# Kernel optimization log

Measured on AMD Instinct MI355X. Metric: run time of the kernel, lower is better.

The kernel has to match this reference:

```python
import jax, jax.numpy as jnp
import numpy as np

BN_EPS = 1e-5
L2_EPS = 1e-8


def l2norm(x, axis=-1):
    # matches torch: x / (sqrt(sum(x^2)) + eps)
    n = jnp.sqrt(jnp.sum(x * x, axis=axis, keepdims=True)) + L2_EPS
    return x / n


def setup_inputs() -> dict:
    key = jax.random.key(0)
    ks = jax.random.split(key, 8)
    B, N, D, E = 512, 193, 512, 2048
    g = 4                      # uniform pid-group size (<= max_rows=8)
    k_tok = (N - 1) // 2       # = 96, matches DynamicLinearProjection k
    H = E // 2                 # MLP hidden = 1024
    base_features = jax.random.normal(ks[0], (B, N, D), jnp.float32)
    atten = jax.random.uniform(ks[1], (B, N, N), jnp.float32)
    pid = jnp.arange(B) // g   # contiguous groups of size g
    # dynamic projection params for group size g
    W_dyn = jax.random.normal(ks[2], (g, D), jnp.float32)          # weights[f'weight_{g}'] ~ randn
    b_dyn = jnp.zeros((g,), jnp.float32)
    W_lin = jax.random.normal(ks[3], (E, k_tok * g), jnp.float32) * 0.02  # linears[f'linear_{g}']
    b_lin = jnp.zeros((E,), jnp.float32)
    # MLP(input=512, hidden=1024, output=2048, 2 layers)
    W1 = jax.random.normal(ks[4], (H, D), jnp.float32) * 0.02
    b1 = jnp.zeros((H,), jnp.float32)
    gamma1 = jnp.ones((H,), jnp.float32)
    beta1 = jnp.zeros((H,), jnp.float32)
    W2 = jax.random.normal(ks[5], (E, H), jnp.float32) * 0.02
    b2 = jnp.zeros((E,), jnp.float32)
    return {"base_features": base_features, "atten": atten, "pid": pid,
            "W_dyn": W_dyn, "b_dyn": b_dyn, "W_lin": W_lin, "b_lin": b_lin,
            "W1": W1, "b1": b1, "gamma1": gamma1, "beta1": beta1,
            "W2": W2, "b2": b2}


def reference(base_features, atten, pid, W_dyn, b_dyn, W_lin, b_lin,
              W1, b1, gamma1, beta1, W2, b2):
    B, N, D = base_features.shape
    k_tok = (N - 1) // 2                      # 96
    g = W_dyn.shape[0]                        # uniform group size (pid = arange//g)
    G = B // g
    E = W_lin.shape[0]
    # --- top-k token selection (atten[:, :, 0] = -1, then topk over atten[:, 0, :]) ---
    scores = atten[:, 0, :].at[:, 0].set(-1.0)            # (B, N)
    _, idx = jax.lax.top_k(scores, k_tok)                 # (B, k_tok), descending
    feats = jnp.take_along_axis(base_features, idx[:, :, None], axis=1)  # (B, k_tok, D)
    # --- per-pid-group dynamic projection (uniform groups -> one batched GEMM) ---
    # torch: cat group members -> (g*k_tok, D); F.linear(x, W_dyn, b_dyn).T -> (g, g*k_tok); linear_g -> (g, E)
    Xg = feats.reshape(G, g * k_tok, D)
    y = jnp.einsum('gnd,rd->grn', Xg, W_dyn) + b_dyn[None, :, None]     # (G, g, g*k_tok)
    new_feats = jnp.einsum('gri,oi->gro', y, W_lin) + b_lin             # (G, g, E)
    # scatter: output[member_idx] = row; contiguous groups => plain reshape
    new_feats = l2norm(new_feats.reshape(B, E))
    # --- MLP branch on l2-normalized selected features ---
    x = l2norm(feats).reshape(B * k_tok, D)
    h = x @ W1.T + b1
    mu = jnp.mean(h, axis=0)
    var = jnp.var(h, axis=0)                  # biased, as torch BN training-mode
    h = (h - mu) * jax.lax.rsqrt(var + BN_EPS) * gamma1 + beta1
    h = jax.nn.relu(h)
    out = (h @ W2.T + b2).reshape(B, k_tok, E)
    pooled = jnp.max(out, axis=1)             # maxk_pool1d_var with k=1 => max over tokens
    return (pooled + new_feats).astype(jnp.float32)
```

## Files before the change

kernel.cpp:

```cpp
#include <hip/hip_runtime.h>
#include <math.h>

#define B_   512
#define N_   193
#define D_   512
#define E_   2048
#define KTOK 96
#define H_   1024
#define M1   (B_ * KTOK)
#define KGD  (KTOK * 4)

typedef _Float16 half8 __attribute__((ext_vector_type(8)));
typedef _Float16 half4v __attribute__((ext_vector_type(4)));
typedef float floatx4 __attribute__((ext_vector_type(4)));

__device__ __forceinline__ void gll16(const _Float16* g, _Float16* l) {
    __builtin_amdgcn_global_load_lds(
        (const __attribute__((address_space(1))) unsigned int*)(const void*)g,
        (__attribute__((address_space(3))) unsigned int*)(void*)l, 16, 0, 0);
}

__global__ void zero_stats_kernel(double* stats) {
    int i = blockIdx.x * 256 + threadIdx.x;
    if (i < 2 * H_) stats[i] = 0.0;
}

__global__ void topk_kernel(const float* __restrict__ atten, int* __restrict__ idx) {
    __shared__ float s[N_];
    int b = blockIdx.x;
    const float* row = atten + (size_t)b * N_ * N_;
    for (int i = threadIdx.x; i < N_; i += blockDim.x)
        s[i] = (i == 0) ? -1.0f : row[i];
    __syncthreads();
    for (int i = threadIdx.x; i < N_; i += blockDim.x) {
        float v = s[i];
        int rank = 0;
        for (int j = 0; j < N_; ++j) {
            float u = s[j];
            rank += (u > v) || (u == v && j < i);
        }
        if (rank < KTOK) idx[b * KTOK + rank] = i;
    }
}

__global__ __launch_bounds__(256) void gather_kernel(
        const float* __restrict__ base, const int* __restrict__ idx,
        const float* __restrict__ W_dyn, const float* __restrict__ b_dyn,
        _Float16* __restrict__ Xh, float* __restrict__ Y) {
    int ln = threadIdx.x & 63, wv = threadIdx.x >> 6;
    int rowid = blockIdx.x * 4 + wv;
    int b = rowid / KTOK, t = rowid - b * KTOK;
    int tok = idx[rowid];
    const float4* src = (const float4*)(base + ((size_t)b * N_ + tok) * D_);
    float4 v0 = src[ln * 2], v1 = src[ln * 2 + 1];

    float vals[5];
    vals[0] = v0.x * v0.x + v0.y * v0.y + v0.z * v0.z + v0.w * v0.w
            + v1.x * v1.x + v1.y * v1.y + v1.z * v1.z + v1.w * v1.w;
#pragma unroll
    for (int r = 0; r < 4; ++r) {
        const float4* wr = (const float4*)(W_dyn + r * D_);
        float4 w0 = wr[ln * 2], w1 = wr[ln * 2 + 1];
        vals[1 + r] = v0.x * w0.x + v0.y * w0.y + v0.z * w0.z + v0.w * w0.w
                    + v1.x * w1.x + v1.y * w1.y + v1.z * w1.z + v1.w * w1.w;
    }
#pragma unroll
    for (int c = 0; c < 5; ++c)
#pragma unroll
        for (int o = 32; o > 0; o >>= 1) vals[c] += __shfl_xor(vals[c], o, 64);

    float inv = 1.0f / (sqrtf(vals[0]) + 1e-8f);
    half8 o8;
    o8[0] = (_Float16)(v0.x * inv); o8[1] = (_Float16)(v0.y * inv);
    o8[2] = (_Float16)(v0.z * inv); o8[3] = (_Float16)(v0.w * inv);
    o8[4] = (_Float16)(v1.x * inv); o8[5] = (_Float16)(v1.y * inv);
    o8[6] = (_Float16)(v1.z * inv); o8[7] = (_Float16)(v1.w * inv);
    *(half8*)&Xh[(size_t)rowid * D_ + ln * 8] = o8;
    if (ln == 0) {
        int g = b >> 2;
        int n = (b & 3) * KTOK + t;
#pragma unroll
        for (int r = 0; r < 4; ++r)
            Y[(size_t)(g * 4 + r) * KGD + n] = vals[1 + r] + b_dyn[r];
    }
}

__global__ __launch_bounds__(256) void newfeat_kernel(
        const float* __restrict__ Y, const float* __restrict__ W_lin,
        const float* __restrict__ b_lin, float* __restrict__ NF) {
    __shared__ float sy[4][KGD];
    __shared__ float red[4][4];
    __shared__ float tot[4];
    int b0 = blockIdx.x * 4;
    int tid = threadIdx.x;
    for (int l = tid; l < 4 * KGD; l += 256)
        sy[l / KGD][l % KGD] = Y[(size_t)b0 * KGD + l];
    __syncthreads();

    float out[4][8];
    float ssq[4] = {0.f, 0.f, 0.f, 0.f};
#pragma unroll
    for (int q = 0; q < 8; ++q) {
        int o = tid + 256 * q;
        float a0 = 0.f, a1 = 0.f, a2 = 0.f, a3 = 0.f;
        const float4* wr = (const float4*)(W_lin + (size_t)o * KGD);
        for (int i4 = 0; i4 < KGD / 4; ++i4) {
            float4 w  = wr[i4];
            float4 s0 = *(const float4*)&sy[0][i4 * 4];
            float4 s1 = *(const float4*)&sy[1][i4 * 4];
            float4 s2 = *(const float4*)&sy[2][i4 * 4];
            float4 s3 = *(const float4*)&sy[3][i4 * 4];
            a0 += w.x * s0.x + w.y * s0.y + w.z * s0.z + w.w * s0.w;
            a1 += w.x * s1.x + w.y * s1.y + w.z * s1.z + w.w * s1.w;
            a2 += w.x * s2.x + w.y * s2.y + w.z * s2.z + w.w * s2.w;
            a3 += w.x * s3.x + w.y * s3.y + w.z * s3.z + w.w * s3.w;
        }
        float bl = b_lin[o];
        out[0][q] = a0 + bl; out[1][q] = a1 + bl;
        out[2][q] = a2 + bl; out[3][q] = a3 + bl;
#pragma unroll
        for (int r = 0; r < 4; ++r) ssq[r] += out[r][q] * out[r][q];
    }

    int lane = tid & 63, wid = tid >> 6;
#pragma unroll
    for (int c = 0; c < 4; ++c) {
        float v = ssq[c];
        for (int o = 32; o > 0; o >>= 1) v += __shfl_down(v, o, 64);
        if (lane == 0) red[c][wid] = v;
    }
    __syncthreads();
    if (tid < 4) tot[tid] = red[tid][0] + red[tid][1] + red[tid][2] + red[tid][3];
    __syncthreads();
#pragma unroll
    for (int r = 0; r < 4; ++r) {
        float norm = sqrtf(tot[r]) + 1e-8f;
#pragma unroll
        for (int q = 0; q < 8; ++q) {
            int o = tid + 256 * q;
            NF[(size_t)(b0 + r) * E_ + o] = out[r][q] / norm;
        }
    }
}

__global__ __launch_bounds__(256) void convw_kernel(
        const float* __restrict__ W1, const float* __restrict__ W2,
        _Float16* __restrict__ W1h, _Float16* __restrict__ W2h) {
    int i = blockIdx.x * 256 + threadIdx.x;
    if (i < 131072) {
        float4 v = *(const float4*)&W1[(size_t)i * 4];
        half4v o = {(_Float16)v.x, (_Float16)v.y, (_Float16)v.z, (_Float16)v.w};
        *(half4v*)&W1h[(size_t)i * 4] = o;
    } else {
        int j = i - 131072;
        float4 v = *(const float4*)&W2[(size_t)j * 4];
        half4v o = {(_Float16)v.x, (_Float16)v.y, (_Float16)v.z, (_Float16)v.w};
        *(half4v*)&W2h[(size_t)j * 4] = o;
    }
}

__global__ __launch_bounds__(512, 2) void gemm1s(
        const _Float16* __restrict__ A, const _Float16* __restrict__ Bm,
        const float* __restrict__ bias, _Float16* __restrict__ Cf16,
        double* __restrict__ stats) {
    constexpr int KA = 512, NS = 16, NBX = 4;
    __shared__ _Float16 Sl[4][14336];
    int tid = threadIdx.x;
    int ln = tid & 63, w = tid >> 6;
    int wr = w >> 2, wc = w & 3;
    int rid = blockIdx.x;
    int q = rid >> 3;
    int bx = q & (NBX - 1);
    int by = ((q / NBX) << 3) | (rid & 7);
    int n0 = bx * 256, m0 = by * 192;

    bool isA = (w < 4);
    const _Float16* sg[4];
    int ld[4];
    if (isA) {
#pragma unroll
        for (int i = 0; i < 3; ++i) {
            int j = w * 3 + i;
            int u = j * 64 + ln;
            int kg = u / 192, row = u - kg * 192;
            sg[i] = A + (size_t)(m0 + row) * KA + kg * 8;
            ld[i] = j * 512;
        }
        sg[3] = sg[0]; ld[3] = ld[0];
    } else {
#pragma unroll
        for (int i = 0; i < 4; ++i) {
            int j = (w - 4) * 4 + i;
            int u = j * 64 + ln;
            int kg = u >> 8, col = u & 255;
            sg[i] = Bm + (size_t)(n0 + col) * KA + kg * 8;
            ld[i] = 6144 + j * 512;
        }
    }

#define CSTAGE(s) { int ko = (s) * 32; _Float16* dst = &Sl[(s) & 3][0];        \
    if (isA) { gll16(sg[0] + ko, dst + ld[0]); gll16(sg[1] + ko, dst + ld[1]); \
               gll16(sg[2] + ko, dst + ld[2]); }                               \
    else     { gll16(sg[0] + ko, dst + ld[0]); gll16(sg[1] + ko, dst + ld[1]); \
               gll16(sg[2] + ko, dst + ld[2]); gll16(sg[3] + ko, dst + ld[3]); } }
#define WAITV(na, nb) { if (isA) asm volatile("s_waitcnt vmcnt(" #na ")" ::: "memory"); \
                        else     asm volatile("s_waitcnt vmcnt(" #nb ")" ::: "memory"); }

    int aofs[6], bofs[4];
#pragma unroll
    for (int f = 0; f < 6; ++f)
        aofs[f] = ((ln >> 4) * 192 + wr * 96 + f * 16 + (ln & 15)) * 8;
#pragma unroll
    for (int n = 0; n < 4; ++n)
        bofs[n] = 6144 + ((ln >> 4) * 256 + wc * 64 + n * 16 + (ln & 15)) * 8;

    floatx4 zero = {0.f, 0.f, 0.f, 0.f};
    floatx4 acc[6][4];
#pragma unroll
    for (int i = 0; i < 6; ++i)
#pragma unroll
        for (int j = 0; j < 4; ++j) acc[i][j] = zero;

    CSTAGE(0); CSTAGE(1); CSTAGE(2);
    WAITV(6, 8);
    __builtin_amdgcn_s_barrier();

    for (int s = 0; s < NS; ++s) {
        const _Float16* SL = &Sl[s & 3][0];
        half8 bv[4], av[3];
#pragma unroll
        for (int n = 0; n < 4; ++n) bv[n] = *(const half8*)&SL[bofs[n]];
#pragma unroll
        for (int f = 0; f < 3; ++f) av[f] = *(const half8*)&SL[aofs[f]];
        if (s + 3 < NS) CSTAGE(s + 3);
        __builtin_amdgcn_sched_barrier(0);
        __builtin_amdgcn_s_barrier();
        asm volatile("s_waitcnt lgkmcnt(0)" ::: "memory");
        __builtin_amdgcn_sched_barrier(0);
        __builtin_amdgcn_s_setprio(1);
#pragma unroll
        for (int f = 0; f < 3; ++f)
#pragma unroll
            for (int n = 0; n < 4; ++n)
                acc[f][n] = __builtin_amdgcn_mfma_f32_16x16x32_f16(av[f], bv[n], acc[f][n], 0, 0, 0);
        __builtin_amdgcn_s_setprio(0);
        __builtin_amdgcn_sched_barrier(0);
        __builtin_amdgcn_s_barrier();
        half8 av2[3];
#pragma unroll
        for (int f = 0; f < 3; ++f) av2[f] = *(const half8*)&SL[aofs[3 + f]];
        __builtin_amdgcn_sched_barrier(0);
        if (s + 1 < NS) {
            if (s + 3 < NS)      { WAITV(6, 8); }
            else if (s + 2 < NS) { WAITV(3, 4); }
            else                 { WAITV(0, 0); }
        }
        __builtin_amdgcn_s_barrier();
        asm volatile("s_waitcnt lgkmcnt(0)" ::: "memory");
        __builtin_amdgcn_sched_barrier(0);
        __builtin_amdgcn_s_setprio(1);
#pragma unroll
        for (int f = 0; f < 3; ++f)
#pragma unroll
            for (int n = 0; n < 4; ++n)
                acc[3 + f][n] = __builtin_amdgcn_mfma_f32_16x16x32_f16(av2[f], bv[n], acc[3 + f][n], 0, 0, 0);
        __builtin_amdgcn_s_setprio(0);
        __builtin_amdgcn_sched_barrier(0);
        __builtin_amdgcn_s_barrier();
    }
#undef CSTAGE
#undef WAITV

    float cs[4] = {0.f, 0.f, 0.f, 0.f}, cq[4] = {0.f, 0.f, 0.f, 0.f};
#pragma unroll
    for (int f = 0; f < 6; ++f) {
        int row = m0 + wr * 96 + f * 16 + (ln >> 4) * 4;
#pragma unroll
        for (int n = 0; n < 4; ++n) {
            int col = n0 + wc * 64 + n * 16 + (ln & 15);
            float bb = bias[col];
#pragma unroll
            for (int r = 0; r < 4; ++r) {
                float v = acc[f][n][r] + bb;
                Cf16[(size_t)(row + r) * H_ + col] = (_Float16)v;
                cs[n] += v; cq[n] += v * v;
            }
        }
    }
#pragma unroll
    for (int n = 0; n < 4; ++n) {
        cs[n] += __shfl_xor(cs[n], 16); cs[n] += __shfl_xor(cs[n], 32);
        cq[n] += __shfl_xor(cq[n], 16); cq[n] += __shfl_xor(cq[n], 32);
    }
    float* sp = (float*)&Sl[0][0];
    if (ln < 16) {
#pragma unroll
        for (int n = 0; n < 4; ++n) {
            int c = wc * 64 + n * 16 + ln;
            sp[(wr * 256 + c) * 2 + 0] = cs[n];
            sp[(wr * 256 + c) * 2 + 1] = cq[n];
        }
    }
    __syncthreads();
    if (tid < 256) {
        float s0 = sp[tid * 2]     + sp[(256 + tid) * 2];
        float q0 = sp[tid * 2 + 1] + sp[(256 + tid) * 2 + 1];
        atomicAdd(&stats[n0 + tid], (double)s0);
        atomicAdd(&stats[H_ + n0 + tid], (double)q0);
    }
}

__global__ void finalize_kernel(const double* __restrict__ stats,
                                const float* __restrict__ gamma,
                                const float* __restrict__ beta,
                                _Float16* __restrict__ scsh16) {
    int c = blockIdx.x * 256 + threadIdx.x;
    if (c >= H_) return;
    double mean = stats[c] / (double)M1;
    double var  = stats[H_ + c] / (double)M1 - mean * mean;
    float sc = gamma[c] * (float)(1.0 / sqrt(var + 1e-5));
    float sh = beta[c] - (float)mean * sc;
    scsh16[c] = (_Float16)sc;
    scsh16[H_ + c] = (_Float16)sh;
}

__device__ __forceinline__ half8 bnrelu8(half8 h, const _Float16* scp, const _Float16* shp) {
    half8 s = *(const half8*)scp, t = *(const half8*)shp, o;
#pragma unroll
    for (int e = 0; e < 8; ++e) {
        float v = (float)h[e] * (float)s[e] + (float)t[e];
        o[e] = (_Float16)fmaxf(v, 0.f);
    }
    return o;
}

__global__ __launch_bounds__(512, 2) void gemm2f(
        const _Float16* __restrict__ Hb, const _Float16* __restrict__ Bm,
        const _Float16* __restrict__ scsh16, const float* __restrict__ bias,
        const float* __restrict__ NF, float* __restrict__ out) {
    constexpr int KA = 1024, NS = 32, NBX = 8;
    __shared__ _Float16 Sl[4][14336];
    __shared__ _Float16 scL[H_], shL[H_];
    int tid = threadIdx.x;
    int ln = tid & 63, w = tid >> 6;
    int wr = w >> 2, wc = w & 3;
    int rid = blockIdx.x;
    int qq = rid >> 3;
    int bx = qq & (NBX - 1);
    int by = ((qq / NBX) << 3) | (rid & 7);
    int n0 = bx * 256, m0 = by * 192;
    bool isA = (w < 4);

    for (int i = tid; i < H_; i += 512) { scL[i] = scsh16[i]; shL[i] = scsh16[H_ + i]; }

    const _Float16 *sgA0 = Hb, *sgA1 = Hb, *sgA2 = Hb;
    int ldA0 = 0, ldA1 = 0, ldA2 = 0, kgA0 = 0, kgA1 = 0, kgA2 = 0;
    const _Float16* sgB[4] = {Bm, Bm, Bm, Bm};
    int ldB[4] = {6144, 6144, 6144, 6144};
    if (isA) {
        { int j = w * 3 + 0; int u = j * 64 + ln; kgA0 = u / 192; int row = u - kgA0 * 192;
          sgA0 = Hb + (size_t)(m0 + row) * KA + kgA0 * 8; ldA0 = j * 512; }
        { int j = w * 3 + 1; int u = j * 64 + ln; kgA1 = u / 192; int row = u - kgA1 * 192;
          sgA1 = Hb + (size_t)(m0 + row) * KA + kgA1 * 8; ldA1 = j * 512; }
        { int j = w * 3 + 2; int u = j * 64 + ln; kgA2 = u / 192; int row = u - kgA2 * 192;
          sgA2 = Hb + (size_t)(m0 + row) * KA + kgA2 * 8; ldA2 = j * 512; }
    } else {
#pragma unroll
        for (int i = 0; i < 4; ++i) {
            int j = (w - 4) * 4 + i;
            int u = j * 64 + ln;
            int kg = u >> 8, col = u & 255;
            sgB[i] = Bm + (size_t)(n0 + col) * KA + kg * 8;
            ldB[i] = 6144 + j * 512;
        }
    }

#define A_ISSUE(t, Ra, Rb, Rc) { Ra = *(const half8*)(sgA0 + (size_t)(t) * 32); \
    Rb = *(const half8*)(sgA1 + (size_t)(t) * 32);                              \
    Rc = *(const half8*)(sgA2 + (size_t)(t) * 32); }
#define A_XFRM(t, Ra, Rb, Rc) { _Float16* dst = &Sl[(t) & 3][0]; int c0 = (t) * 32; \
    *(half8*)(dst + ldA0 + ln * 8) = bnrelu8(Ra, &scL[c0 + kgA0 * 8], &shL[c0 + kgA0 * 8]); \
    *(half8*)(dst + ldA1 + ln * 8) = bnrelu8(Rb, &scL[c0 + kgA1 * 8], &shL[c0 + kgA1 * 8]); \
    *(half8*)(dst + ldA2 + ln * 8) = bnrelu8(Rc, &scL[c0 + kgA2 * 8], &shL[c0 + kgA2 * 8]); }
#define B_STAGE(t) { int ko = (t) * 32; _Float16* dst = &Sl[(t) & 3][0]; \
    gll16(sgB[0] + ko, dst + ldB[0]); gll16(sgB[1] + ko, dst + ldB[1]); \
    gll16(sgB[2] + ko, dst + ldB[2]); gll16(sgB[3] + ko, dst + ldB[3]); }

    int aofs[6], bofs[4];
#pragma unroll
    for (int f = 0; f < 6; ++f)
        aofs[f] = ((ln >> 4) * 192 + wr * 96 + f * 16 + (ln & 15)) * 8;
#pragma unroll
    for (int n = 0; n < 4; ++n)
        bofs[n] = 6144 + ((ln >> 4) * 256 + wc * 64 + n * 16 + (ln & 15)) * 8;

    floatx4 zero = {0.f, 0.f, 0.f, 0.f};
    floatx4 acc[6][4];
#pragma unroll
    for (int i = 0; i < 6; ++i)
#pragma unroll
        for (int j = 0; j < 4; ++j) acc[i][j] = zero;

    half8 e0a, e0b, e0c, e1a, e1b, e1c;

    if (isA) { A_ISSUE(0, e0a, e0b, e0c); A_ISSUE(1, e1a, e1b, e1c); }
    else     { B_STAGE(0); B_STAGE(1); B_STAGE(2); }
    asm volatile("s_waitcnt lgkmcnt(0)" ::: "memory");
    __builtin_amdgcn_s_barrier();
    if (isA) {
        A_XFRM(0, e0a, e0b, e0c);
        A_ISSUE(2, e0a, e0b, e0c);
        A_XFRM(1, e1a, e1b, e1c);
    } else {
        asm volatile("s_waitcnt vmcnt(8)" ::: "memory");
    }
    asm volatile("s_waitcnt lgkmcnt(0)" ::: "memory");
    __builtin_amdgcn_s_barrier();

#define SLOT(s, Ia, Ib, Ic, Xa, Xb, Xc) {                                       \
    const _Float16* SL = &Sl[(s) & 3][0];                                       \
    half8 bv[4], av[3], av2[3];                                                 \
    _Pragma("unroll") for (int n = 0; n < 4; ++n) bv[n] = *(const half8*)&SL[bofs[n]]; \
    _Pragma("unroll") for (int f = 0; f < 3; ++f) av[f] = *(const half8*)&SL[aofs[f]]; \
    if ((s) + 3 < NS) { if (isA) { A_ISSUE((s) + 3, Ia, Ib, Ic); } else { B_STAGE((s) + 3); } } \
    __builtin_amdgcn_sched_barrier(0);                                          \
    __builtin_amdgcn_s_barrier();                                               \
    asm volatile("s_waitcnt lgkmcnt(0)" ::: "memory");                          \
    __builtin_amdgcn_sched_barrier(0);                                          \
    __builtin_amdgcn_s_setprio(1);                                              \
    _Pragma("unroll") for (int f = 0; f < 3; ++f)                               \
        _Pragma("unroll") for (int n = 0; n < 4; ++n)                           \
            acc[f][n] = __builtin_amdgcn_mfma_f32_16x16x32_f16(av[f], bv[n], acc[f][n], 0, 0, 0); \
    __builtin_amdgcn_s_setprio(0);                                              \
    __builtin_amdgcn_sched_barrier(0);                                          \
    __builtin_amdgcn_s_barrier();                                               \
    _Pragma("unroll") for (int f = 0; f < 3; ++f) av2[f] = *(const half8*)&SL[aofs[3 + f]]; \
    __builtin_amdgcn_sched_barrier(0);                                          \
    __builtin_amdgcn_s_barrier();                                               \
    asm volatile("s_waitcnt lgkmcnt(0)" ::: "memory");                          \
    __builtin_amdgcn_sched_barrier(0);                                          \
    __builtin_amdgcn_s_setprio(1);                                              \
    _Pragma("unroll") for (int f = 0; f < 3; ++f)                               \
        _Pragma("unroll") for (int n = 0; n < 4; ++n)                           \
            acc[3 + f][n] = __builtin_amdgcn_mfma_f32_16x16x32_f16(av2[f], bv[n], acc[3 + f][n], 0, 0, 0); \
    __builtin_amdgcn_s_setprio(0);                                              \
    __builtin_amdgcn_sched_barrier(0);                                          \
    if (isA) {                                                                  \
        if ((s) + 2 < NS) { A_XFRM((s) + 2, Xa, Xb, Xc); }                      \
    } else {                                                                    \
        if ((s) + 3 < NS)      { asm volatile("s_waitcnt vmcnt(8)" ::: "memory"); } \
        else if ((s) + 2 < NS) { asm volatile("s_waitcnt vmcnt(4)" ::: "memory"); } \
        else if ((s) + 1 < NS) { asm volatile("s_waitcnt vmcnt(0)" ::: "memory"); } \
    }                                                                           \
    __builtin_amdgcn_s_barrier();                                               \
}

    for (int s = 0; s < NS; s += 2) {
        SLOT(s,     e1a, e1b, e1c, e0a, e0b, e0c);
        SLOT(s + 1, e0a, e0b, e0c, e1a, e1b, e1c);
    }
#undef SLOT
#undef A_ISSUE
#undef A_XFRM
#undef B_STAGE

    int batch = by * 2 + wr;
#pragma unroll
    for (int n = 0; n < 4; ++n) {
        float m = -3.4e38f;
#pragma unroll
        for (int f = 0; f < 6; ++f)
#pragma unroll
            for (int r = 0; r < 4; ++r) m = fmaxf(m, acc[f][n][r]);
        m = fmaxf(m, __shfl_xor(m, 16));
        m = fmaxf(m, __shfl_xor(m, 32));
        if (ln < 16) {
            int col = n0 + wc * 64 + n * 16 + ln;
            out[(size_t)batch * E_ + col] = m + bias[col] + NF[(size_t)batch * E_ + col];
        }
    }
}

extern "C" void kernel_launch(void* const* d_in, const int* in_sizes, int n_in,
                              void* d_out, int out_size, void* d_ws, size_t ws_size,
                              hipStream_t stream) {
    (void)in_sizes; (void)n_in; (void)out_size; (void)ws_size;
    const float* base  = (const float*)d_in[0];
    const float* atten = (const float*)d_in[1];
    const float* W_dyn = (const float*)d_in[3];
    const float* b_dyn = (const float*)d_in[4];
    const float* W_lin = (const float*)d_in[5];
    const float* b_lin = (const float*)d_in[6];
    const float* W1    = (const float*)d_in[7];
    const float* b1    = (const float*)d_in[8];
    const float* gamma = (const float*)d_in[9];
    const float* beta  = (const float*)d_in[10];
    const float* W2    = (const float*)d_in[11];
    const float* b2    = (const float*)d_in[12];
    float* out = (float*)d_out;

    char* wsp = (char*)d_ws;
    int*      idx    = (int*)(wsp);
    float*    Y      = (float*)(wsp + 196608);
    float*    NF     = (float*)(wsp + 983040);
    double*   stats  = (double*)(wsp + 5177344);
    _Float16* scsh16 = (_Float16*)(wsp + 5193728);
    _Float16* W1h    = (_Float16*)(wsp + 5201920);
    _Float16* W2h    = (_Float16*)(wsp + 6250496);
    _Float16* Xh     = (_Float16*)(wsp + 10444800);
    _Float16* Hbh    = (_Float16*)(wsp + 60776448);

    zero_stats_kernel<<<8, 256, 0, stream>>>(stats);
    topk_kernel<<<B_, 256, 0, stream>>>(atten, idx);
    convw_kernel<<<2560, 256, 0, stream>>>(W1, W2, W1h, W2h);
    gather_kernel<<<M1 / 4, 256, 0, stream>>>(base, idx, W_dyn, b_dyn, Xh, Y);
    newfeat_kernel<<<B_ / 4, 256, 0, stream>>>(Y, W_lin, b_lin, NF);
    gemm1s<<<1024, 512, 0, stream>>>(Xh, W1h, b1, Hbh, stats);
    finalize_kernel<<<4, 256, 0, stream>>>(stats, gamma, beta, scsh16);
    gemm2f<<<2048, 512, 0, stream>>>(Hbh, W2h, scsh16, b2, NF, out);
}
```

Measured before the change: 542.0 us.

## Switch both GEMMs to double-buffered BK=64 stages with all-warp loading

Both GEMM kernels move from a 4-slot, 32-wide K pipeline with three stages in flight to a 2-slot, 64-wide K double buffer. In gemm1s all warps now share the global-to-LDS loads rather than splitting them into A-loader and B-loader warps. Each iteration runs two MFMA halves with fewer barriers, so there is less synchronisation per K step. The cost is a shallower prefetch: each iteration ends with a full vmcnt(0) wait, which may expose global memory latency.

```diff
diff --git a/kernel.cpp b/kernel.cpp
--- a/kernel.cpp
+++ b/kernel.cpp
@@ -159,12 +159,13 @@
     }
 }
 
+
 __global__ __launch_bounds__(512, 2) void gemm1s(
         const _Float16* __restrict__ A, const _Float16* __restrict__ Bm,
         const float* __restrict__ bias, _Float16* __restrict__ Cf16,
         double* __restrict__ stats) {
-    constexpr int KA = 512, NS = 16, NBX = 4;
-    __shared__ _Float16 Sl[4][14336];
+    constexpr int KA = 512, NS = 8, NBX = 4;
+    __shared__ _Float16 Sl[2][28672];
     int tid = threadIdx.x;
     int ln = tid & 63, w = tid >> 6;
     int wr = w >> 2, wc = w & 3;
@@ -174,45 +175,37 @@
     int by = ((q / NBX) << 3) | (rid & 7);
     int n0 = bx * 256, m0 = by * 192;
 
-    bool isA = (w < 4);
-    const _Float16* sg[4];
-    int ld[4];
-    if (isA) {
-#pragma unroll
-        for (int i = 0; i < 3; ++i) {
-            int j = w * 3 + i;
-            int u = j * 64 + ln;
+    const _Float16* sg[7];
+    int ld[7];
+#pragma unroll
+    for (int i = 0; i < 7; ++i) {
+        int c = w * 7 + i;
+        if (c < 24) {
+            int u = c * 64 + ln;
             int kg = u / 192, row = u - kg * 192;
             sg[i] = A + (size_t)(m0 + row) * KA + kg * 8;
-            ld[i] = j * 512;
-        }
-        sg[3] = sg[0]; ld[3] = ld[0];
-    } else {
-#pragma unroll
-        for (int i = 0; i < 4; ++i) {
-            int j = (w - 4) * 4 + i;
-            int u = j * 64 + ln;
+            ld[i] = c * 512;
+        } else {
+            int u = (c - 24) * 64 + ln;
             int kg = u >> 8, col = u & 255;
             sg[i] = Bm + (size_t)(n0 + col) * KA + kg * 8;
-            ld[i] = 6144 + j * 512;
-        }
-    }
-
-#define CSTAGE(s) { int ko = (s) * 32; _Float16* dst = &Sl[(s) & 3][0];        \
-    if (isA) { gll16(sg[0] + ko, dst + ld[0]); gll16(sg[1] + ko, dst + ld[1]); \
-               gll16(sg[2] + ko, dst + ld[2]); }                               \
-    else     { gll16(sg[0] + ko, dst + ld[0]); gll16(sg[1] + ko, dst + ld[1]); \
-               gll16(sg[2] + ko, dst + ld[2]); gll16(sg[3] + ko, dst + ld[3]); } }
-#define WAITV(na, nb) { if (isA) asm volatile("s_waitcnt vmcnt(" #na ")" ::: "memory"); \
-                        else     asm volatile("s_waitcnt vmcnt(" #nb ")" ::: "memory"); }
-
-    int aofs[6], bofs[4];
+            ld[i] = 12288 + (c - 24) * 512;
+        }
+    }
+#define G1STAGE(t) { int ko = (t) * 64; _Float16* dst = &Sl[(t) & 1][0];      \
+    _Pragma("unroll") for (int i = 0; i < 7; ++i) gll16(sg[i] + ko, dst + ld[i]); }
+
+    int aofs[6][2], bofs[4][2];
 #pragma unroll
     for (int f = 0; f < 6; ++f)
-        aofs[f] = ((ln >> 4) * 192 + wr * 96 + f * 16 + (ln & 15)) * 8;
+#pragma unroll
+        for (int h = 0; h < 2; ++h)
+            aofs[f][h] = ((h * 4 + (ln >> 4)) * 192 + wr * 96 + f * 16 + (ln & 15)) * 8;
 #pragma unroll
     for (int n = 0; n < 4; ++n)
-        bofs[n] = 6144 + ((ln >> 4) * 256 + wc * 64 + n * 16 + (ln & 15)) * 8;
+#pragma unroll
+        for (int h = 0; h < 2; ++h)
+            bofs[n][h] = 12288 + ((h * 4 + (ln >> 4)) * 256 + wc * 64 + n * 16 + (ln & 15)) * 8;
 
     floatx4 zero = {0.f, 0.f, 0.f, 0.f};
     floatx4 acc[6][4];
@@ -221,55 +214,48 @@
 #pragma unroll
         for (int j = 0; j < 4; ++j) acc[i][j] = zero;
 
-    CSTAGE(0); CSTAGE(1); CSTAGE(2);
-    WAITV(6, 8);
+    G1STAGE(0);
+    asm volatile("s_waitcnt vmcnt(0)" ::: "memory");
     __builtin_amdgcn_s_barrier();
 
     for (int s = 0; s < NS; ++s) {
-        const _Float16* SL = &Sl[s & 3][0];
-        half8 bv[4], av[3];
-#pragma unroll
-        for (int n = 0; n < 4; ++n) bv[n] = *(const half8*)&SL[bofs[n]];
-#pragma unroll
-        for (int f = 0; f < 3; ++f) av[f] = *(const half8*)&SL[aofs[f]];
-        if (s + 3 < NS) CSTAGE(s + 3);
-        __builtin_amdgcn_sched_barrier(0);
-        __builtin_amdgcn_s_barrier();
+        const _Float16* SL = &Sl[s & 1][0];
+        half8 a0[6], b0[4];
+#pragma unroll
+        for (int n = 0; n < 4; ++n) b0[n] = *(const half8*)&SL[bofs[n][0]];
+#pragma unroll
+        for (int f = 0; f < 6; ++f) a0[f] = *(const half8*)&SL[aofs[f][0]];
+        if (s + 1 < NS) G1STAGE(s + 1);
         asm volatile("s_waitcnt lgkmcnt(0)" ::: "memory");
         __builtin_amdgcn_sched_barrier(0);
         __builtin_amdgcn_s_setprio(1);
 #pragma unroll
-        for (int f = 0; f < 3; ++f)
+        for (int f = 0; f < 6; ++f)
 #pragma unroll
             for (int n = 0; n < 4; ++n)
-                acc[f][n] = __builtin_amdgcn_mfma_f32_16x16x32_f16(av[f], bv[n], acc[f][n], 0, 0, 0);
+                acc[f][n] = __builtin_amdgcn_mfma_f32_16x16x32_f16(a0[f], b0[n], acc[f][n], 0, 0, 0);
         __builtin_amdgcn_s_setprio(0);
+        {
+            half8 a1[6], b1[4];
+#pragma unroll
+            for (int n = 0; n < 4; ++n) b1[n] = *(const half8*)&SL[bofs[n][1]];
+#pragma unroll
+            for (int f = 0; f < 6; ++f) a1[f] = *(const half8*)&SL[aofs[f][1]];
+            asm volatile("s_waitcnt lgkmcnt(0)" ::: "memory");
+            __builtin_amdgcn_sched_barrier(0);
+            __builtin_amdgcn_s_setprio(1);
+#pragma unroll
+            for (int f = 0; f < 6; ++f)
+#pragma unroll
+                for (int n = 0; n < 4; ++n)
+                    acc[f][n] = __builtin_amdgcn_mfma_f32_16x16x32_f16(a1[f], b1[n], acc[f][n], 0, 0, 0);
+            __builtin_amdgcn_s_setprio(0);
+        }
         __builtin_amdgcn_sched_barrier(0);
+        asm volatile("s_waitcnt vmcnt(0)" ::: "memory");
         __builtin_amdgcn_s_barrier();
-        half8 av2[3];
-#pragma unroll
-        for (int f = 0; f < 3; ++f) av2[f] = *(const half8*)&SL[aofs[3 + f]];
-        __builtin_amdgcn_sched_barrier(0);
-        if (s + 1 < NS) {
-            if (s + 3 < NS)      { WAITV(6, 8); }
-            else if (s + 2 < NS) { WAITV(3, 4); }
-            else                 { WAITV(0, 0); }
-        }
-        __builtin_amdgcn_s_barrier();
-        asm volatile("s_waitcnt lgkmcnt(0)" ::: "memory");
-        __builtin_amdgcn_sched_barrier(0);
-        __builtin_amdgcn_s_setprio(1);
-#pragma unroll
-        for (int f = 0; f < 3; ++f)
-#pragma unroll
-            for (int n = 0; n < 4; ++n)
-                acc[3 + f][n] = __builtin_amdgcn_mfma_f32_16x16x32_f16(av2[f], bv[n], acc[3 + f][n], 0, 0, 0);
-        __builtin_amdgcn_s_setprio(0);
-        __builtin_amdgcn_sched_barrier(0);
-        __builtin_amdgcn_s_barrier();
-    }
-#undef CSTAGE
-#undef WAITV
+    }
+#undef G1STAGE
 
     float cs[4] = {0.f, 0.f, 0.f, 0.f}, cq[4] = {0.f, 0.f, 0.f, 0.f};
 #pragma unroll
@@ -338,8 +324,8 @@
         const _Float16* __restrict__ Hb, const _Float16* __restrict__ Bm,
         const _Float16* __restrict__ scsh16, const float* __restrict__ bias,
         const float* __restrict__ NF, float* __restrict__ out) {
-    constexpr int KA = 1024, NS = 32, NBX = 8;
-    __shared__ _Float16 Sl[4][14336];
+    constexpr int KA = 1024, NS = 16, NBX = 8;
+    __shared__ _Float16 Sl[2][28672];
     __shared__ _Float16 scL[H_], shL[H_];
     int tid = threadIdx.x;
     int ln = tid & 63, w = tid >> 6;
@@ -353,46 +339,53 @@
 
     for (int i = tid; i < H_; i += 512) { scL[i] = scsh16[i]; shL[i] = scsh16[H_ + i]; }
 
-    const _Float16 *sgA0 = Hb, *sgA1 = Hb, *sgA2 = Hb;
-    int ldA0 = 0, ldA1 = 0, ldA2 = 0, kgA0 = 0, kgA1 = 0, kgA2 = 0;
-    const _Float16* sgB[4] = {Bm, Bm, Bm, Bm};
-    int ldB[4] = {6144, 6144, 6144, 6144};
+    const _Float16* sgA[6];
+    int ldA[6], cgA[6];
+    half8 ar[6];
     if (isA) {
-        { int j = w * 3 + 0; int u = j * 64 + ln; kgA0 = u / 192; int row = u - kgA0 * 192;
-          sgA0 = Hb + (size_t)(m0 + row) * KA + kgA0 * 8; ldA0 = j * 512; }
-        { int j = w * 3 + 1; int u = j * 64 + ln; kgA1 = u / 192; int row = u - kgA1 * 192;
-          sgA1 = Hb + (size_t)(m0 + row) * KA + kgA1 * 8; ldA1 = j * 512; }
-        { int j = w * 3 + 2; int u = j * 64 + ln; kgA2 = u / 192; int row = u - kgA2 * 192;
-          sgA2 = Hb + (size_t)(m0 + row) * KA + kgA2 * 8; ldA2 = j * 512; }
-    } else {
-#pragma unroll
-        for (int i = 0; i < 4; ++i) {
-            int j = (w - 4) * 4 + i;
-            int u = j * 64 + ln;
+#pragma unroll
+        for (int i = 0; i < 6; ++i) {
+            int c = w * 6 + i;
+            int u = c * 64 + ln;
+            int kg = u / 192, row = u - kg * 192;
+            sgA[i] = Hb + (size_t)(m0 + row) * KA + kg * 8;
+            ldA[i] = c * 512;
+            cgA[i] = kg;
+        }
+    }
+    const _Float16* sgB[8];
+    int ldB[8];
+    if (!isA) {
+#pragma unroll
+        for (int i = 0; i < 8; ++i) {
+            int c = (w - 4) * 8 + i;
+            int u = c * 64 + ln;
             int kg = u >> 8, col = u & 255;
             sgB[i] = Bm + (size_t)(n0 + col) * KA + kg * 8;
-            ldB[i] = 6144 + j * 512;
-        }
-    }
-
-#define A_ISSUE(t, Ra, Rb, Rc) { Ra = *(const half8*)(sgA0 + (size_t)(t) * 32); \
-    Rb = *(const half8*)(sgA1 + (size_t)(t) * 32);                              \
-    Rc = *(const half8*)(sgA2 + (size_t)(t) * 32); }
-#define A_XFRM(t, Ra, Rb, Rc) { _Float16* dst = &Sl[(t) & 3][0]; int c0 = (t) * 32; \
-    *(half8*)(dst + ldA0 + ln * 8) = bnrelu8(Ra, &scL[c0 + kgA0 * 8], &shL[c0 + kgA0 * 8]); \
-    *(half8*)(dst + ldA1 + ln * 8) = bnrelu8(Rb, &scL[c0 + kgA1 * 8], &shL[c0 + kgA1 * 8]); \
-    *(half8*)(dst + ldA2 + ln * 8) = bnrelu8(Rc, &scL[c0 + kgA2 * 8], &shL[c0 + kgA2 * 8]); }
-#define B_STAGE(t) { int ko = (t) * 32; _Float16* dst = &Sl[(t) & 3][0]; \
-    gll16(sgB[0] + ko, dst + ldB[0]); gll16(sgB[1] + ko, dst + ldB[1]); \
-    gll16(sgB[2] + ko, dst + ldB[2]); gll16(sgB[3] + ko, dst + ldB[3]); }
-
-    int aofs[6], bofs[4];
+            ldB[i] = 12288 + c * 512;
+        }
+    }
+
+#define A_ISSUE(t) { _Pragma("unroll") for (int i = 0; i < 6; ++i)            \
+    ar[i] = *(const half8*)(sgA[i] + (size_t)(t) * 64); }
+#define A_XFRM(t) { _Float16* dst = &Sl[(t) & 1][0];                          \
+    _Pragma("unroll") for (int i = 0; i < 6; ++i) {                           \
+        int c0 = (t) * 64 + cgA[i] * 8;                                       \
+        *(half8*)(dst + ldA[i] + ln * 8) = bnrelu8(ar[i], &scL[c0], &shL[c0]); } }
+#define B_STAGE(t) { int ko = (t) * 64; _Float16* dst = &Sl[(t) & 1][0];      \
+    _Pragma("unroll") for (int i = 0; i < 8; ++i) gll16(sgB[i] + ko, dst + ldB[i]); }
+
+    int aofs[6][2], bofs[4][2];
 #pragma unroll
     for (int f = 0; f < 6; ++f)
-        aofs[f] = ((ln >> 4) * 192 + wr * 96 + f * 16 + (ln & 15)) * 8;
+#pragma unroll
+        for (int h = 0; h < 2; ++h)
+            aofs[f][h] = ((h * 4 + (ln >> 4)) * 192 + wr * 96 + f * 16 + (ln & 15)) * 8;
 #pragma unroll
     for (int n = 0; n < 4; ++n)
-        bofs[n] = 6144 + ((ln >> 4) * 256 + wc * 64 + n * 16 + (ln & 15)) * 8;
+#pragma unroll
+        for (int h = 0; h < 2; ++h)
+            bofs[n][h] = 12288 + ((h * 4 + (ln >> 4)) * 256 + wc * 64 + n * 16 + (ln & 15)) * 8;
 
     floatx4 zero = {0.f, 0.f, 0.f, 0.f};
     floatx4 acc[6][4];
@@ -401,65 +394,51 @@
 #pragma unroll
         for (int j = 0; j < 4; ++j) acc[i][j] = zero;
 
-    half8 e0a, e0b, e0c, e1a, e1b, e1c;
-
-    if (isA) { A_ISSUE(0, e0a, e0b, e0c); A_ISSUE(1, e1a, e1b, e1c); }
-    else     { B_STAGE(0); B_STAGE(1); B_STAGE(2); }
+    if (isA) { A_ISSUE(0); } else { B_STAGE(0); }
     asm volatile("s_waitcnt lgkmcnt(0)" ::: "memory");
     __builtin_amdgcn_s_barrier();
-    if (isA) {
-        A_XFRM(0, e0a, e0b, e0c);
-        A_ISSUE(2, e0a, e0b, e0c);
-        A_XFRM(1, e1a, e1b, e1c);
-    } else {
-        asm volatile("s_waitcnt vmcnt(8)" ::: "memory");
-    }
-    asm volatile("s_waitcnt lgkmcnt(0)" ::: "memory");
+    if (isA) { A_XFRM(0); }
+    asm volatile("s_waitcnt lgkmcnt(0) vmcnt(0)" ::: "memory");
     __builtin_amdgcn_s_barrier();
 
-#define SLOT(s, Ia, Ib, Ic, Xa, Xb, Xc) {                                       \
-    const _Float16* SL = &Sl[(s) & 3][0];                                       \
-    half8 bv[4], av[3], av2[3];                                                 \
-    _Pragma("unroll") for (int n = 0; n < 4; ++n) bv[n] = *(const half8*)&SL[bofs[n]]; \
-    _Pragma("unroll") for (int f = 0; f < 3; ++f) av[f] = *(const half8*)&SL[aofs[f]]; \
-    if ((s) + 3 < NS) { if (isA) { A_ISSUE((s) + 3, Ia, Ib, Ic); } else { B_STAGE((s) + 3); } } \
-    __builtin_amdgcn_sched_barrier(0);                                          \
-    __builtin_amdgcn_s_barrier();                                               \
-    asm volatile("s_waitcnt lgkmcnt(0)" ::: "memory");                          \
-    __builtin_amdgcn_sched_barrier(0);                                          \
-    __builtin_amdgcn_s_setprio(1);                                              \
-    _Pragma("unroll") for (int f = 0; f < 3; ++f)                               \
-        _Pragma("unroll") for (int n = 0; n < 4; ++n)                           \
-            acc[f][n] = __builtin_amdgcn_mfma_f32_16x16x32_f16(av[f], bv[n], acc[f][n], 0, 0, 0); \
-    __builtin_amdgcn_s_setprio(0);                                              \
-    __builtin_amdgcn_sched_barrier(0);                                          \
-    __builtin_amdgcn_s_barrier();                                               \
-    _Pragma("unroll") for (int f = 0; f < 3; ++f) av2[f] = *(const half8*)&SL[aofs[3 + f]]; \
-    __builtin_amdgcn_sched_barrier(0);                                          \
-    __builtin_amdgcn_s_barrier();                                               \
-    asm volatile("s_waitcnt lgkmcnt(0)" ::: "memory");                          \
-    __builtin_amdgcn_sched_barrier(0);                                          \
-    __builtin_amdgcn_s_setprio(1);                                              \
-    _Pragma("unroll") for (int f = 0; f < 3; ++f)                               \
-        _Pragma("unroll") for (int n = 0; n < 4; ++n)                           \
-            acc[3 + f][n] = __builtin_amdgcn_mfma_f32_16x16x32_f16(av2[f], bv[n], acc[3 + f][n], 0, 0, 0); \
-    __builtin_amdgcn_s_setprio(0);                                              \
-    __builtin_amdgcn_sched_barrier(0);                                          \
-    if (isA) {                                                                  \
-        if ((s) + 2 < NS) { A_XFRM((s) + 2, Xa, Xb, Xc); }                      \
-    } else {                                                                    \
-        if ((s) + 3 < NS)      { asm volatile("s_waitcnt vmcnt(8)" ::: "memory"); } \
-        else if ((s) + 2 < NS) { asm volatile("s_waitcnt vmcnt(4)" ::: "memory"); } \
-        else if ((s) + 1 < NS) { asm volatile("s_waitcnt vmcnt(0)" ::: "memory"); } \
-    }                                                                           \
-    __builtin_amdgcn_s_barrier();                                               \
-}
-
-    for (int s = 0; s < NS; s += 2) {
-        SLOT(s,     e1a, e1b, e1c, e0a, e0b, e0c);
-        SLOT(s + 1, e0a, e0b, e0c, e1a, e1b, e1c);
-    }
-#undef SLOT
+    for (int s = 0; s < NS; ++s) {
+        const _Float16* SL = &Sl[s & 1][0];
+        half8 a0[6], b0[4];
+#pragma unroll
+        for (int n = 0; n < 4; ++n) b0[n] = *(const half8*)&SL[bofs[n][0]];
+#pragma unroll
+        for (int f = 0; f < 6; ++f) a0[f] = *(const half8*)&SL[aofs[f][0]];
+        if (s + 1 < NS) { if (isA) { A_ISSUE(s + 1); } else { B_STAGE(s + 1); } }
+        asm volatile("s_waitcnt lgkmcnt(0)" ::: "memory");
+        __builtin_amdgcn_sched_barrier(0);
+        __builtin_amdgcn_s_setprio(1);
+#pragma unroll
+        for (int f = 0; f < 6; ++f)
+#pragma unroll
+            for (int n = 0; n < 4; ++n)
+                acc[f][n] = __builtin_amdgcn_mfma_f32_16x16x32_f16(a0[f], b0[n], acc[f][n], 0, 0, 0);
+        __builtin_amdgcn_s_setprio(0);
+        {
+            half8 a1[6], b1[4];
+#pragma unroll
+            for (int n = 0; n < 4; ++n) b1[n] = *(const half8*)&SL[bofs[n][1]];
+#pragma unroll
+            for (int f = 0; f < 6; ++f) a1[f] = *(const half8*)&SL[aofs[f][1]];
+            asm volatile("s_waitcnt lgkmcnt(0)" ::: "memory");
+            __builtin_amdgcn_sched_barrier(0);
+            __builtin_amdgcn_s_setprio(1);
+#pragma unroll
+            for (int f = 0; f < 6; ++f)
+#pragma unroll
+                for (int n = 0; n < 4; ++n)
+                    acc[f][n] = __builtin_amdgcn_mfma_f32_16x16x32_f16(a1[f], b1[n], acc[f][n], 0, 0, 0);
+            __builtin_amdgcn_s_setprio(0);
+        }
+        __builtin_amdgcn_sched_barrier(0);
+        if (s + 1 < NS && isA) { A_XFRM(s + 1); }
+        asm volatile("s_waitcnt lgkmcnt(0) vmcnt(0)" ::: "memory");
+        __builtin_amdgcn_s_barrier();
+    }
 #undef A_ISSUE
 #undef A_XFRM
 #undef B_STAGE
```

Result: slower. 606.9 us (+12.0%).
